# Kernel optimization log

Hardware: AMD Instinct MI355X
Metric: run time of the kernel (lower is better)

## Reference

```python
import jax, jax.numpy as jnp
import numpy as np

NUM_ROUNDS = 64
D_HIDDEN = 256
B = 16384

# MD5 message schedule g(i)
_SCHED = np.array([i if i < 16 else ((5*i+1) % 16 if i < 32 else ((3*i+5) % 16 if i < 48 else (7*i) % 16)) for i in range(64)], dtype=np.int32)
# MD5 per-round shift amounts
_SHIFT = np.array([7,12,17,22]*4 + [5,9,14,20]*4 + [4,11,16,23]*4 + [6,10,15,21]*4, dtype=np.float32)
# round_info[i] = [i/64, shift[i]/25], shape (64, 2)
_ROUND_INFO = np.stack([np.arange(64, dtype=np.float32) / 64.0, _SHIFT / 25.0], axis=-1)


def setup_inputs() -> dict:
    key = jax.random.key(0)
    ks = jax.random.split(key, 8)
    return {
        "message_bytes": jax.random.uniform(ks[0], (B, 64), dtype=jnp.float32),
        "initial_state": jax.random.uniform(ks[1], (B, 16), dtype=jnp.float32),
        "W1": jax.random.normal(ks[2], (NUM_ROUNDS, 22, D_HIDDEN), dtype=jnp.float32) * (1.0 / np.sqrt(22.0)),
        "b1": jax.random.normal(ks[3], (NUM_ROUNDS, D_HIDDEN), dtype=jnp.float32) * 0.02,
        "W2": jax.random.normal(ks[4], (NUM_ROUNDS, D_HIDDEN, D_HIDDEN), dtype=jnp.float32) * (1.0 / np.sqrt(float(D_HIDDEN))),
        "b2": jax.random.normal(ks[5], (NUM_ROUNDS, D_HIDDEN), dtype=jnp.float32) * 0.02,
        "W3": jax.random.normal(ks[6], (NUM_ROUNDS, D_HIDDEN, 16), dtype=jnp.float32) * (1.0 / np.sqrt(float(D_HIDDEN))),
        "b3": jax.random.normal(ks[7], (NUM_ROUNDS, 16), dtype=jnp.float32) * 0.02,
    }


def reference(message_bytes, initial_state, W1, b1, W2, b2, W3, b3):
    Bsz = message_bytes.shape[0]
    msg_words = message_bytes.reshape(Bsz, 16, 4)
    # pre-gather the scheduled word per round: (64, B, 4)
    words = jnp.transpose(msg_words[:, jnp.asarray(_SCHED), :], (1, 0, 2))
    round_info = jnp.asarray(_ROUND_INFO)  # (64, 2)

    def step(state, xs):
        word, rinfo, w1, c1, w2, c2, w3, c3 = xs
        x = jnp.concatenate([state, word, jnp.broadcast_to(rinfo, (state.shape[0], 2))], axis=-1)  # (B, 22)
        h = jax.nn.gelu(x @ w1 + c1, approximate=False)
        h = jax.nn.gelu(h @ w2 + c2, approximate=False)
        return h @ w3 + c3, None

    final_state, _ = jax.lax.scan(step, initial_state, (words, round_info, W1, b1, W2, b2, W3, b3))
    return final_state
```

## Files before the change

### kernel.cpp

```cpp
#include <hip/hip_runtime.h>
#include <stdint.h>


using bf16x8   = __attribute__((ext_vector_type(8))) __bf16;
using floatx4  = __attribute__((ext_vector_type(4))) float;
using ushort4v = __attribute__((ext_vector_type(4))) unsigned short;

__constant__ int c_sched[64] = {
  0,1,2,3,4,5,6,7,8,9,10,11,12,13,14,15,
  1,6,11,0,5,10,15,4,9,14,3,8,13,2,7,12,
  5,8,11,14,1,4,7,10,13,0,3,6,9,12,15,2,
  0,7,14,5,12,3,10,1,8,15,6,13,4,11,2,9
};
__constant__ float c_shift[64] = {
  7,12,17,22,7,12,17,22,7,12,17,22,7,12,17,22,
  5,9,14,20,5,9,14,20,5,9,14,20,5,9,14,20,
  4,11,16,23,4,11,16,23,4,11,16,23,4,11,16,23,
  6,10,15,21,6,10,15,21,6,10,15,21,6,10,15,21
};

__device__ __forceinline__ unsigned short bfbits(__bf16 b) {
  union { __bf16 b; unsigned short u; } v; v.b = b; return v.u;
}
__device__ __forceinline__ float gelu_f(float x) {
  float ax = fabsf(x);
  float t  = __builtin_amdgcn_rcpf(__builtin_fmaf(0.33270222f, ax, 1.0f));
  float e  = __builtin_amdgcn_exp2f(x * x * -0.72134752f);
  float poly = t * __builtin_fmaf(t, __builtin_fmaf(t, 0.7478556f, -0.0958798f),
                                  0.3480242f);
  float er = __builtin_fmaf(-poly, e, 1.0f);
  er = copysignf(er, x);
  float hx = 0.5f * x;
  return __builtin_fmaf(hx, er, hx);
}
__device__ __forceinline__ floatx4 mfma16(bf16x8 a, bf16x8 b, floatx4 c) {
  return __builtin_amdgcn_mfma_f32_16x16x32_bf16(a, b, c, 0, 0, 0);
}
struct BfPair { unsigned short h, l; };
__device__ __forceinline__ BfPair split2(float s) {
  __bf16 hb = (__bf16)s;
  __bf16 lb = (__bf16)(s - (float)hb);
  BfPair p; p.h = bfbits(hb); p.l = bfbits(lb); return p;
}

#define N1G (64*16*64)
#define N2G (64*16*8*64)
#define N3G (64*8*64)

__global__ void pack_w(const float* __restrict__ W1,
                       const float* __restrict__ W2,
                       const float* __restrict__ W3,
                       unsigned short* __restrict__ P) {
  int gid = blockIdx.x * blockDim.x + threadIdx.x;
  if (gid >= N1G + N2G + N3G) return;
  unsigned short v[8];
  unsigned short* dst;
  if (gid < N1G) {
    int lane = gid & 63, t = (gid >> 6) & 15, r = gid >> 10;
    int qq = lane >> 4, mm = lane & 15;
    #pragma unroll
    for (int j = 0; j < 8; ++j) {
      int k = 8*qq + j;
      v[j] = (k < 22) ? bfbits((__bf16)W1[(r*22 + k)*256 + 16*t + mm]) : (unsigned short)0;
    }
    dst = P + (size_t)gid * 8;
  } else if (gid < N1G + N2G) {
    int g = gid - N1G;
    int lane = g & 63, c = (g >> 6) & 7, t = (g >> 9) & 15, r = g >> 13;
    int qq = lane >> 4, mm = lane & 15;
    #pragma unroll
    for (int j = 0; j < 8; ++j) {
      int k = 32*c + 8*qq + j;
      v[j] = bfbits((__bf16)W2[((size_t)r*256 + k)*256 + 16*t + mm]);
    }
    dst = P + (size_t)(N1G + g) * 8;
  } else {
    int g = gid - N1G - N2G;
    int lane = g & 63, c = (g >> 6) & 7, r = g >> 9;
    int qq = lane >> 4, mm = lane & 15;
    #pragma unroll
    for (int j = 0; j < 8; ++j) {
      int k = 32*c + 8*qq + j;
      v[j] = bfbits((__bf16)W3[(r*256 + k)*16 + mm]);
    }
    dst = P + (size_t)(N1G + N2G + g) * 8;
  }
  ushort4v lo = { v[0],v[1],v[2],v[3] }, hi = { v[4],v[5],v[6],v[7] };
  *(ushort4v*)dst = lo;
  *(ushort4v*)(dst + 4) = hi;
}

#define NG  2
#define SXW 36
#define SH 264
#define SM 66

__global__ __launch_bounds__(256, 2) void md5_main(
    const float* __restrict__ msg,
    const float* __restrict__ st0,
    const float* __restrict__ b1,
    const float* __restrict__ b2,
    const float* __restrict__ b3,
    const unsigned short* __restrict__ P,
    float* __restrict__ out)
{
  __shared__ unsigned short xh[4][NG][16][SXW], xl[4][NG][16][SXW];
  __shared__ unsigned short hA[NG][16][SH], hB[NG][16][SH];
  __shared__ unsigned short msgb[NG*16][SM], msgl[NG*16][SM];

  const int tid  = threadIdx.x;
  const int wv   = tid >> 6;
  const int lane = tid & 63;
  const int q    = lane >> 4;
  const int ln   = lane & 15;
  const int row0 = blockIdx.x * (NG*16);

  const unsigned short* P1 = P;
  const unsigned short* P2 = P + (size_t)N1G * 8;
  const unsigned short* P3 = P + (size_t)(N1G + N2G) * 8;

  for (int i = lane; i < NG*16*SXW; i += 64) {
    (&xh[wv][0][0][0])[i] = 0; (&xl[wv][0][0][0])[i] = 0;
  }
  {
    int idx = tid * 8, rr = idx >> 6, cc = idx & 63;
    floatx4 v0 = *(const floatx4*)(msg + (size_t)(row0 + rr)*64 + cc);
    floatx4 v1 = *(const floatx4*)(msg + (size_t)(row0 + rr)*64 + cc + 4);
    #pragma unroll
    for (int j = 0; j < 4; ++j) {
      BfPair p0 = split2(v0[j]);
      BfPair p1 = split2(v1[j]);
      msgb[rr][cc + j]     = p0.h;  msgl[rr][cc + j]     = p0.l;
      msgb[rr][cc + 4 + j] = p1.h;  msgl[rr][cc + 4 + j] = p1.l;
    }
  }
  #pragma unroll
  for (int g = 0; g < NG; ++g) {
    floatx4 v = *(const floatx4*)(st0 + (size_t)(row0 + g*16 + ln)*16 + 4*q);
    ushort4v h4, l4;
    #pragma unroll
    for (int e = 0; e < 4; ++e) { BfPair p = split2(v[e]); h4[e] = p.h; l4[e] = p.l; }
    *(ushort4v*)&xh[wv][g][ln][4*q] = h4;
    *(ushort4v*)&xl[wv][g][ln][4*q] = l4;
  }
  __syncthreads();
  if (lane < NG*16) {
    int g = lane >> 4, n = lane & 15, rrow = lane;
    int s = c_sched[0];
    BfPair i1p = split2(c_shift[0] / 25.0f);
    #pragma unroll
    for (int j = 0; j < 4; ++j) {
      xh[wv][g][n][16+j] = msgb[rrow][4*s+j];
      xl[wv][g][n][16+j] = msgl[rrow][4*s+j];
    }
    xh[wv][g][n][20] = 0;     xl[wv][g][n][20] = 0;
    xh[wv][g][n][21] = i1p.h; xl[wv][g][n][21] = i1p.l;
  }

  #pragma unroll 1
  for (int r = 0; r < 64; ++r) {
    floatx4 bb1[4];
    bf16x8  a1[4];
    const unsigned short* p1 = P1 + ((size_t)(r*16 + 4*wv)*64 + lane)*8;
    #pragma unroll
    for (int tt = 0; tt < 4; ++tt) {
      a1[tt]  = *(const bf16x8*)(p1 + (size_t)tt*512);
      bb1[tt] = *(const floatx4*)(b1 + r*256 + (4*wv + tt)*16 + 4*q);
    }
    bf16x8 bxh[NG], bxl[NG];
    #pragma unroll
    for (int g = 0; g < NG; ++g) {
      bxh[g] = *(const bf16x8*)&xh[wv][g][ln][8*q];
      bxl[g] = *(const bf16x8*)&xl[wv][g][ln][8*q];
    }
    #pragma unroll
    for (int tt = 0; tt < 4; ++tt) {
      int f0 = (4*wv + tt)*16 + 4*q;
      #pragma unroll
      for (int g = 0; g < NG; ++g) {
        floatx4 acc = bb1[tt];
        acc = mfma16(a1[tt], bxl[g], acc);
        acc = mfma16(a1[tt], bxh[g], acc);
        ushort4v h4;
        #pragma unroll
        for (int e = 0; e < 4; ++e) h4[e] = bfbits((__bf16)gelu_f(acc[e]));
        *(ushort4v*)&hA[g][ln][f0] = h4;
      }
    }
    __syncthreads();

    bf16x8 a3[8];
    {
      const unsigned short* p3 = P3 + ((size_t)(r*8)*64 + lane)*8;
      #pragma unroll
      for (int c = 0; c < 8; ++c) a3[c] = *(const bf16x8*)(p3 + (size_t)c*512);
    }
    floatx4 bb3 = *(const floatx4*)(b3 + r*16 + 4*q);
    floatx4 bb2[4];
    #pragma unroll
    for (int tt = 0; tt < 4; ++tt)
      bb2[tt] = *(const floatx4*)(b2 + r*256 + (4*wv + tt)*16 + 4*q);

    bf16x8 Bf[NG][8];
    #pragma unroll
    for (int g = 0; g < NG; ++g)
      #pragma unroll
      for (int c = 0; c < 8; ++c) Bf[g][c] = *(const bf16x8*)&hA[g][ln][32*c + 8*q];

    const unsigned short* p2 = P2 + ((size_t)((r*16 + 4*wv)*8)*64 + lane)*8;
    #pragma unroll
    for (int tt = 0; tt < 4; ++tt) {
      bf16x8 a2[8];
      #pragma unroll
      for (int c = 0; c < 8; ++c)
        a2[c] = *(const bf16x8*)(p2 + (size_t)(tt*8 + c)*512);
      int f0 = (4*wv + tt)*16 + 4*q;
      #pragma unroll
      for (int g = 0; g < NG; ++g) {
        floatx4 acc = bb2[tt];
        #pragma unroll
        for (int c = 0; c < 8; ++c) acc = mfma16(a2[c], Bf[g][c], acc);
        ushort4v h4;
        #pragma unroll
        for (int e = 0; e < 4; ++e) h4[e] = bfbits((__bf16)gelu_f(acc[e]));
        *(ushort4v*)&hB[g][ln][f0] = h4;
      }
    }
    __syncthreads();

    #pragma unroll
    for (int g = 0; g < NG; ++g) {
      floatx4 s = bb3;
      #pragma unroll
      for (int c = 0; c < 8; ++c) {
        bf16x8 bh = *(const bf16x8*)&hB[g][ln][32*c + 8*q];
        s = mfma16(a3[c], bh, s);
      }
      if (r == 63) {
        if (wv == 0)
          *(floatx4*)(out + (size_t)(row0 + g*16 + ln)*16 + 4*q) = s;
      } else {
        ushort4v h4, l4;
        #pragma unroll
        for (int e = 0; e < 4; ++e) { BfPair p = split2(s[e]); h4[e] = p.h; l4[e] = p.l; }
        *(ushort4v*)&xh[wv][g][ln][4*q] = h4;
        *(ushort4v*)&xl[wv][g][ln][4*q] = l4;
      }
    }
    if (lane < NG*16 && r < 63) {
      int g = lane >> 4, n = lane & 15, rrow = lane;
      int sc = c_sched[r+1];
      float i0 = (float)(r+1) * 0.015625f;
      BfPair i1p = split2(c_shift[r+1] / 25.0f);
      #pragma unroll
      for (int j = 0; j < 4; ++j) {
        xh[wv][g][n][16+j] = msgb[rrow][4*sc+j];
        xl[wv][g][n][16+j] = msgl[rrow][4*sc+j];
      }
      xh[wv][g][n][20] = bfbits((__bf16)i0); xl[wv][g][n][20] = 0;
      xh[wv][g][n][21] = i1p.h;              xl[wv][g][n][21] = i1p.l;
    }
  }
}

extern "C" void kernel_launch(void* const* d_in, const int* in_sizes, int n_in,
                              void* d_out, int out_size, void* d_ws, size_t ws_size,
                              hipStream_t stream) {
  const float* msg = (const float*)d_in[0];
  const float* st0 = (const float*)d_in[1];
  const float* W1  = (const float*)d_in[2];
  const float* b1  = (const float*)d_in[3];
  const float* W2  = (const float*)d_in[4];
  const float* b2  = (const float*)d_in[5];
  const float* W3  = (const float*)d_in[6];
  const float* b3  = (const float*)d_in[7];
  float* out = (float*)d_out;
  (void)in_sizes; (void)n_in; (void)out_size; (void)ws_size;

  unsigned short* P = (unsigned short*)d_ws;
  const int totalGroups = N1G + N2G + N3G;
  pack_w<<<(totalGroups + 255) / 256, 256, 0, stream>>>(W1, W2, W3, P);
  md5_main<<<512, 256, 0, stream>>>(msg, st0, b1, b2, b3, P, out);
}
```

Baseline: 468.5 us.

## Split each block's feature tiles across eight waves and share the state buffer

Blocks grow from 256 to 512 threads. Each wave now computes 2 of the 16-column feature tiles in layers 1 and 2 instead of 4, and the per-wave private copies of the round input state are merged into one shared buffer. The aim is more waves per block to hide latency and less per-wave work between barriers. In exchange, all eight waves still compute layer 3 redundantly and write identical values into the shared state buffer. The tighter launch bound also lowers the register budget, which may cause spilling of the large bf16 fragment arrays.

```diff
diff --git a/kernel.cpp b/kernel.cpp
--- a/kernel.cpp
+++ b/kernel.cpp
@@ -91,11 +91,12 @@
 }
 
 #define NG  2
+#define TT  2
 #define SXW 36
 #define SH 264
 #define SM 66
 
-__global__ __launch_bounds__(256, 2) void md5_main(
+__global__ __launch_bounds__(512, 4) void md5_main(
     const float* __restrict__ msg,
     const float* __restrict__ st0,
     const float* __restrict__ b1,
@@ -104,7 +105,7 @@
     const unsigned short* __restrict__ P,
     float* __restrict__ out)
 {
-  __shared__ unsigned short xh[4][NG][16][SXW], xl[4][NG][16][SXW];
+  __shared__ unsigned short xh[NG][16][SXW], xl[NG][16][SXW];
   __shared__ unsigned short hA[NG][16][SH], hB[NG][16][SH];
   __shared__ unsigned short msgb[NG*16][SM], msgl[NG*16][SM];
 
@@ -119,29 +120,28 @@
   const unsigned short* P2 = P + (size_t)N1G * 8;
   const unsigned short* P3 = P + (size_t)(N1G + N2G) * 8;
 
-  for (int i = lane; i < NG*16*SXW; i += 64) {
-    (&xh[wv][0][0][0])[i] = 0; (&xl[wv][0][0][0])[i] = 0;
+  for (int i = tid; i < NG*16*SXW; i += 512) {
+    (&xh[0][0][0])[i] = 0; (&xl[0][0][0])[i] = 0;
   }
   {
-    int idx = tid * 8, rr = idx >> 6, cc = idx & 63;
+    int idx = tid * 4, rr = idx >> 6, cc = idx & 63;
     floatx4 v0 = *(const floatx4*)(msg + (size_t)(row0 + rr)*64 + cc);
-    floatx4 v1 = *(const floatx4*)(msg + (size_t)(row0 + rr)*64 + cc + 4);
     #pragma unroll
     for (int j = 0; j < 4; ++j) {
       BfPair p0 = split2(v0[j]);
-      BfPair p1 = split2(v1[j]);
-      msgb[rr][cc + j]     = p0.h;  msgl[rr][cc + j]     = p0.l;
-      msgb[rr][cc + 4 + j] = p1.h;  msgl[rr][cc + 4 + j] = p1.l;
-    }
-  }
-  #pragma unroll
-  for (int g = 0; g < NG; ++g) {
-    floatx4 v = *(const floatx4*)(st0 + (size_t)(row0 + g*16 + ln)*16 + 4*q);
-    ushort4v h4, l4;
-    #pragma unroll
-    for (int e = 0; e < 4; ++e) { BfPair p = split2(v[e]); h4[e] = p.h; l4[e] = p.l; }
-    *(ushort4v*)&xh[wv][g][ln][4*q] = h4;
-    *(ushort4v*)&xl[wv][g][ln][4*q] = l4;
+      msgb[rr][cc + j] = p0.h;  msgl[rr][cc + j] = p0.l;
+    }
+  }
+  if (wv == 0) {
+    #pragma unroll
+    for (int g = 0; g < NG; ++g) {
+      floatx4 v = *(const floatx4*)(st0 + (size_t)(row0 + g*16 + ln)*16 + 4*q);
+      ushort4v h4, l4;
+      #pragma unroll
+      for (int e = 0; e < 4; ++e) { BfPair p = split2(v[e]); h4[e] = p.h; l4[e] = p.l; }
+      *(ushort4v*)&xh[g][ln][4*q] = h4;
+      *(ushort4v*)&xl[g][ln][4*q] = l4;
+    }
   }
   __syncthreads();
   if (lane < NG*16) {
@@ -150,32 +150,32 @@
     BfPair i1p = split2(c_shift[0] / 25.0f);
     #pragma unroll
     for (int j = 0; j < 4; ++j) {
-      xh[wv][g][n][16+j] = msgb[rrow][4*s+j];
-      xl[wv][g][n][16+j] = msgl[rrow][4*s+j];
-    }
-    xh[wv][g][n][20] = 0;     xl[wv][g][n][20] = 0;
-    xh[wv][g][n][21] = i1p.h; xl[wv][g][n][21] = i1p.l;
+      xh[g][n][16+j] = msgb[rrow][4*s+j];
+      xl[g][n][16+j] = msgl[rrow][4*s+j];
+    }
+    xh[g][n][20] = 0;     xl[g][n][20] = 0;
+    xh[g][n][21] = i1p.h; xl[g][n][21] = i1p.l;
   }
 
   #pragma unroll 1
   for (int r = 0; r < 64; ++r) {
-    floatx4 bb1[4];
-    bf16x8  a1[4];
-    const unsigned short* p1 = P1 + ((size_t)(r*16 + 4*wv)*64 + lane)*8;
-    #pragma unroll
-    for (int tt = 0; tt < 4; ++tt) {
+    floatx4 bb1[TT];
+    bf16x8  a1[TT];
+    const unsigned short* p1 = P1 + ((size_t)(r*16 + TT*wv)*64 + lane)*8;
+    #pragma unroll
+    for (int tt = 0; tt < TT; ++tt) {
       a1[tt]  = *(const bf16x8*)(p1 + (size_t)tt*512);
-      bb1[tt] = *(const floatx4*)(b1 + r*256 + (4*wv + tt)*16 + 4*q);
+      bb1[tt] = *(const floatx4*)(b1 + r*256 + (TT*wv + tt)*16 + 4*q);
     }
     bf16x8 bxh[NG], bxl[NG];
     #pragma unroll
     for (int g = 0; g < NG; ++g) {
-      bxh[g] = *(const bf16x8*)&xh[wv][g][ln][8*q];
-      bxl[g] = *(const bf16x8*)&xl[wv][g][ln][8*q];
-    }
-    #pragma unroll
-    for (int tt = 0; tt < 4; ++tt) {
-      int f0 = (4*wv + tt)*16 + 4*q;
+      bxh[g] = *(const bf16x8*)&xh[g][ln][8*q];
+      bxl[g] = *(const bf16x8*)&xl[g][ln][8*q];
+    }
+    #pragma unroll
+    for (int tt = 0; tt < TT; ++tt) {
+      int f0 = (TT*wv + tt)*16 + 4*q;
       #pragma unroll
       for (int g = 0; g < NG; ++g) {
         floatx4 acc = bb1[tt];
@@ -196,10 +196,10 @@
       for (int c = 0; c < 8; ++c) a3[c] = *(const bf16x8*)(p3 + (size_t)c*512);
     }
     floatx4 bb3 = *(const floatx4*)(b3 + r*16 + 4*q);
-    floatx4 bb2[4];
-    #pragma unroll
-    for (int tt = 0; tt < 4; ++tt)
-      bb2[tt] = *(const floatx4*)(b2 + r*256 + (4*wv + tt)*16 + 4*q);
+    floatx4 bb2[TT];
+    #pragma unroll
+    for (int tt = 0; tt < TT; ++tt)
+      bb2[tt] = *(const floatx4*)(b2 + r*256 + (TT*wv + tt)*16 + 4*q);
 
     bf16x8 Bf[NG][8];
     #pragma unroll
@@ -207,14 +207,14 @@
       #pragma unroll
       for (int c = 0; c < 8; ++c) Bf[g][c] = *(const bf16x8*)&hA[g][ln][32*c + 8*q];
 
-    const unsigned short* p2 = P2 + ((size_t)((r*16 + 4*wv)*8)*64 + lane)*8;
-    #pragma unroll
-    for (int tt = 0; tt < 4; ++tt) {
+    const unsigned short* p2 = P2 + ((size_t)((r*16 + TT*wv)*8)*64 + lane)*8;
+    #pragma unroll
+    for (int tt = 0; tt < TT; ++tt) {
       bf16x8 a2[8];
       #pragma unroll
       for (int c = 0; c < 8; ++c)
         a2[c] = *(const bf16x8*)(p2 + (size_t)(tt*8 + c)*512);
-      int f0 = (4*wv + tt)*16 + 4*q;
+      int f0 = (TT*wv + tt)*16 + 4*q;
       #pragma unroll
       for (int g = 0; g < NG; ++g) {
         floatx4 acc = bb2[tt];
@@ -243,8 +243,8 @@
         ushort4v h4, l4;
         #pragma unroll
         for (int e = 0; e < 4; ++e) { BfPair p = split2(s[e]); h4[e] = p.h; l4[e] = p.l; }
-        *(ushort4v*)&xh[wv][g][ln][4*q] = h4;
-        *(ushort4v*)&xl[wv][g][ln][4*q] = l4;
+        *(ushort4v*)&xh[g][ln][4*q] = h4;
+        *(ushort4v*)&xl[g][ln][4*q] = l4;
       }
     }
     if (lane < NG*16 && r < 63) {
@@ -254,11 +254,11 @@
       BfPair i1p = split2(c_shift[r+1] / 25.0f);
       #pragma unroll
       for (int j = 0; j < 4; ++j) {
-        xh[wv][g][n][16+j] = msgb[rrow][4*sc+j];
-        xl[wv][g][n][16+j] = msgl[rrow][4*sc+j];
-      }
-      xh[wv][g][n][20] = bfbits((__bf16)i0); xl[wv][g][n][20] = 0;
-      xh[wv][g][n][21] = i1p.h;              xl[wv][g][n][21] = i1p.l;
+        xh[g][n][16+j] = msgb[rrow][4*sc+j];
+        xl[g][n][16+j] = msgl[rrow][4*sc+j];
+      }
+      xh[g][n][20] = bfbits((__bf16)i0); xl[g][n][20] = 0;
+      xh[g][n][21] = i1p.h;              xl[g][n][21] = i1p.l;
     }
   }
 }
@@ -280,5 +280,5 @@
   unsigned short* P = (unsigned short*)d_ws;
   const int totalGroups = N1G + N2G + N3G;
   pack_w<<<(totalGroups + 255) / 256, 256, 0, stream>>>(W1, W2, W3, P);
-  md5_main<<<512, 256, 0, stream>>>(msg, st0, b1, b2, b3, P, out);
-}
+  md5_main<<<512, 512, 0, stream>>>(msg, st0, b1, b2, b3, P, out);
+}
```

Result: slower. 513.0 us (+9.5%).
